# Kernel optimization log

Measured on AMD Instinct MI355X. Metric: run time of the kernel, lower is better.

Reference implementation:

```python
import jax, jax.numpy as jnp
import numpy as np

EPS = 1e-5       # norm_eps
CHUNK = 64       # scan checkpoint chunk size

def _short_conv(x, w):
    # causal depthwise conv (kernel K) + SiLU; x:[B,T,C], w:[C,K]
    K = w.shape[1]
    T = x.shape[1]
    xp = jnp.pad(x, ((0, 0), (K - 1, 0), (0, 0)))
    y = sum(xp[:, i:i + T, :] * w[:, i] for i in range(K))
    return jax.nn.silu(y)

def _l2norm(x):
    return x * jax.lax.rsqrt(jnp.sum(x * x, -1, keepdims=True) + 1e-6)

def _forward(hidden_states, Wq, Wk, Wv, conv_q, conv_k, conv_v, Wf1, Wf2, Wb,
             A_log, dt_bias, Wg, bg, o_norm_w, Wo):
    B, T, _ = hidden_states.shape
    H = A_log.shape[0]
    x = hidden_states
    q = _short_conv(x @ Wq, conv_q)
    k = _short_conv(x @ Wk, conv_k)
    v = _short_conv(x @ Wv, conv_v)
    Dk = q.shape[-1] // H
    Dv = v.shape[-1] // H
    q = _l2norm(q.reshape(B, T, H, Dk))
    k = _l2norm(k.reshape(B, T, H, Dk))
    v = v.reshape(B, T, H, Dv)
    beta = jax.nn.sigmoid(x @ Wb)                               # [B,T,H]
    g = ((x @ Wf1) @ Wf2).reshape(B, T, H, Dk)
    # KDA gate: g = -exp(A_log) * softplus(g + dt_bias), per head & key channel
    g = -jnp.exp(A_log)[:, None] * jax.nn.softplus(g + dt_bias.reshape(H, Dk))
    gexp = jnp.exp(g)                                           # decay in (0,1)
    scale = Dk ** -0.5

    def step(S, inp):
        q_t, k_t, v_t, ge_t, b_t = inp                          # [B,H,Dk]..., [B,H]
        S = S * ge_t[..., None]                                 # per-key-channel decay
        kv = jnp.einsum('bhk,bhkv->bhv', k_t, S)                # current prediction
        upd = (v_t - kv) * b_t[..., None]                       # delta-rule update
        S = S + jnp.einsum('bhk,bhv->bhkv', k_t, upd)
        o_t = jnp.einsum('bhk,bhkv->bhv', q_t, S) * scale
        return S, o_t

    @jax.checkpoint
    def chunk_fn(S, chunk):
        return jax.lax.scan(step, S, chunk)

    def tm(a):  # [B,T,...] -> [T//CHUNK, CHUNK, B, ...]
        a = jnp.moveaxis(a, 1, 0)
        return a.reshape((T // CHUNK, CHUNK) + a.shape[1:])

    S0 = jnp.zeros((B, H, Dk, Dv), dtype=q.dtype)
    _, o = jax.lax.scan(chunk_fn, S0, (tm(q), tm(k), tm(v), tm(gexp), tm(beta)))
    o = jnp.moveaxis(o.reshape((T, B, H, Dv)), 0, 1)            # [B,T,H,Dv]

    gate_o = (x @ Wg + bg).reshape(B, T, H, Dv)
    on = o * jax.lax.rsqrt(jnp.mean(o * o, -1, keepdims=True) + EPS) * o_norm_w
    on = on * jax.nn.silu(gate_o)                               # gated RMSNorm
    return on.reshape(B, T, H * Dv) @ Wo


def setup_inputs() -> dict:
    key = jax.random.key(0)
    ks = jax.random.split(key, 16)
    B, T, D = 2, 2048, 2048
    H, Dk, Dv, K = 16, 128, 128, 4
    n = jax.random.normal
    return {
        'hidden_states': n(ks[0], (B, T, D), jnp.float32),
        'Wq': n(ks[1], (D, H * Dk), jnp.float32) * D ** -0.5,
        'Wk': n(ks[2], (D, H * Dk), jnp.float32) * D ** -0.5,
        'Wv': n(ks[3], (D, H * Dv), jnp.float32) * D ** -0.5,
        'conv_q': n(ks[4], (H * Dk, K), jnp.float32) * 0.5,
        'conv_k': n(ks[5], (H * Dk, K), jnp.float32) * 0.5,
        'conv_v': n(ks[6], (H * Dv, K), jnp.float32) * 0.5,
        'Wf1': n(ks[7], (D, Dv), jnp.float32) * D ** -0.5,
        'Wf2': n(ks[8], (Dv, H * Dk), jnp.float32) * Dv ** -0.5,
        'Wb': n(ks[9], (D, H), jnp.float32) * D ** -0.5,
        'A_log': jnp.log(jax.random.uniform(ks[10], (H,), jnp.float32, 1.0, 16.0)),
        'dt_bias': jnp.zeros((H * Dk,), jnp.float32),
        'Wg': n(ks[11], (D, H * Dv), jnp.float32) * D ** -0.5,
        'bg': jnp.zeros((H * Dv,), jnp.float32),
        'o_norm_w': jnp.ones((Dv,), jnp.float32),
        'Wo': n(ks[12], (H * Dv, D), jnp.float32) * (H * Dv) ** -0.5,
    }


def reference(hidden_states, Wq, Wk, Wv, conv_q, conv_k, conv_v, Wf1, Wf2, Wb,
              A_log, dt_bias, Wg, bg, o_norm_w, Wo):
    return _forward(hidden_states, Wq, Wk, Wv, conv_q, conv_k, conv_v, Wf1, Wf2,
                    Wb, A_log, dt_bias, Wg, bg, o_norm_w, Wo)
```

## Files before the change

### kernel.cpp

```cpp
#include <hip/hip_runtime.h>
#include <stdint.h>

#define BB 2
#define TT 2048
#define DD 2048
#define HH 16
#define HD 2048
#define MM 4096
#define SCH 16

typedef float f32x4 __attribute__((ext_vector_type(4)));
typedef __bf16 bf16x8 __attribute__((ext_vector_type(8)));
typedef unsigned short u16x4 __attribute__((ext_vector_type(4)));
typedef unsigned int u32x4 __attribute__((ext_vector_type(4)));

__device__ __forceinline__ unsigned short f2b(float f) {
  unsigned int u = __float_as_uint(f);
  u += 0x7FFFu + ((u >> 16) & 1u);
  return (unsigned short)(u >> 16);
}

__device__ __forceinline__ void async_ld16(const void* g, void* l) {
  typedef __attribute__((address_space(3))) void as3_t;
  typedef const __attribute__((address_space(1))) void as1_t;
  __builtin_amdgcn_global_load_lds((as1_t*)(uintptr_t)g,
                                   (as3_t*)(unsigned int)(uintptr_t)l, 16, 0, 0);
}

template <int CTRL>
__device__ __forceinline__ float dpp_add(float x) {
  int y = __builtin_amdgcn_update_dpp(0, __float_as_int(x), CTRL, 0xF, 0xF, false);
  return x + __int_as_float(y);
}
__device__ __forceinline__ float reduce16(float x) {
  x = dpp_add<0xB1>(x);
  x = dpp_add<0x4E>(x);
  x = dpp_add<0x124>(x);
  x = dpp_add<0x128>(x);
  return x;
}

__global__ __launch_bounds__(256) void cast_f32_bf16(const float* __restrict__ in,
                                                     unsigned short* __restrict__ out,
                                                     int n4) {
  int i = blockIdx.x * 256 + threadIdx.x;
  if (i >= n4) return;
  f32x4 v = *(const f32x4*)(in + (size_t)i * 4);
  u16x4 r;
  #pragma unroll
  for (int j = 0; j < 4; j++) r[j] = f2b(v[j]);
  *(u16x4*)(out + (size_t)i * 4) = r;
}

__global__ __launch_bounds__(256) void transpose_cast(const float* __restrict__ in,
                                                      unsigned short* __restrict__ out,
                                                      int R, int C) {
  __shared__ float tile[32][33];
  int bx = blockIdx.x * 32, by = blockIdx.y * 32;
  int tx = threadIdx.x, ty = threadIdx.y;
  #pragma unroll
  for (int i = 0; i < 32; i += 8)
    tile[ty + i][tx] = in[(size_t)(by + ty + i) * C + bx + tx];
  __syncthreads();
  #pragma unroll
  for (int i = 0; i < 32; i += 8)
    out[(size_t)(bx + ty + i) * R + by + tx] = f2b(tile[tx][ty + i]);
}

#define GEMM_PROLOGUE_AND_LOOP                                                         \
  __shared__ __align__(16) unsigned short As[128 * 32];                                \
  __shared__ __align__(16) unsigned short Bs[128 * 32];                                \
  int tid = threadIdx.x;                                                               \
  int l = tid & 63, w = tid >> 6;                                                      \
  int nbx = gridDim.x;                                                                 \
  int tot = nbx * gridDim.y;                                                           \
  int id = blockIdx.y * nbx + blockIdx.x;                                              \
  int nid = id;                                                                        \
  if ((tot & 7) == 0) { int per = tot >> 3; nid = (id & 7) * per + (id >> 3); }        \
  int row0 = (nid / nbx) * 128, col0 = (nid % nbx) * 128;                              \
  int wm = (w >> 1) * 64, wn = (w & 1) * 64;                                           \
  const f32x4 fz = {0.f, 0.f, 0.f, 0.f};                                               \
  f32x4 acc[4][4];                                                                     \
  _Pragma("unroll") for (int i = 0; i < 4; i++)                                        \
    _Pragma("unroll") for (int j = 0; j < 4; j++) acc[i][j] = fz;                      \
  int srow = l >> 2, skoff = (l & 3) * 8;                                              \
  int quad = l >> 4, mrow = l & 15;                                                    \
  for (int kt = 0; kt < K; kt += 32) {                                                 \
    _Pragma("unroll") for (int i = 0; i < 2; i++) {                                    \
      int c = w * 2 + i;                                                               \
      const unsigned short* gA = A + (size_t)(row0 + c * 16 + srow) * K + kt + skoff;  \
      const unsigned short* gB = Bt + (size_t)(col0 + c * 16 + srow) * K + kt + skoff; \
      async_ld16(gA, As + c * 512);                                                    \
      async_ld16(gB, Bs + c * 512);                                                    \
    }                                                                                  \
    __syncthreads();                                                                   \
    bf16x8 af[4], bfr[4];                                                              \
    _Pragma("unroll") for (int i = 0; i < 4; i++)                                      \
      af[i] = *(const bf16x8*)(As + (wm + i * 16 + mrow) * 32 + quad * 8);             \
    _Pragma("unroll") for (int j = 0; j < 4; j++)                                      \
      bfr[j] = *(const bf16x8*)(Bs + (wn + j * 16 + mrow) * 32 + quad * 8);            \
    _Pragma("unroll") for (int i = 0; i < 4; i++)                                      \
      _Pragma("unroll") for (int j = 0; j < 4; j++)                                    \
        acc[i][j] = __builtin_amdgcn_mfma_f32_16x16x32_bf16(af[i], bfr[j], acc[i][j],  \
                                                            0, 0, 0);                  \
    __syncthreads();                                                                   \
  }

__global__ __launch_bounds__(256) void gemm_bf16(const unsigned short* __restrict__ A,
                                                 const unsigned short* __restrict__ Bt,
                                                 float* __restrict__ C,
                                                 const float* __restrict__ bias,
                                                 int M, int N, int K) {
  GEMM_PROLOGUE_AND_LOOP
  #pragma unroll
  for (int i = 0; i < 4; i++)
    #pragma unroll
    for (int j = 0; j < 4; j++)
      #pragma unroll
      for (int r = 0; r < 4; r++) {
        int rr = row0 + wm + i * 16 + quad * 4 + r;
        int cc = col0 + wn + j * 16 + mrow;
        float v = acc[i][j][r];
        if (bias) v += bias[cc];
        C[(size_t)rr * N + cc] = v;
      }
}

__global__ __launch_bounds__(256) void gemm_bf16_bout(const unsigned short* __restrict__ A,
                                                      const unsigned short* __restrict__ Bt,
                                                      unsigned short* __restrict__ C,
                                                      const float* __restrict__ bias,
                                                      int M, int N, int K) {
  GEMM_PROLOGUE_AND_LOOP
  #pragma unroll
  for (int i = 0; i < 4; i++)
    #pragma unroll
    for (int j = 0; j < 4; j++)
      #pragma unroll
      for (int r = 0; r < 4; r++) {
        int rr = row0 + wm + i * 16 + quad * 4 + r;
        int cc = col0 + wn + j * 16 + mrow;
        C[(size_t)rr * N + cc] = f2b(acc[i][j][r] + bias[cc]);
      }
}

__global__ __launch_bounds__(256) void gemm_qkv(const unsigned short* __restrict__ A,
                                                const unsigned short* __restrict__ Bt,
                                                unsigned short* __restrict__ Dq,
                                                unsigned short* __restrict__ Dk,
                                                unsigned short* __restrict__ Dv,
                                                int M, int N, int K) {
  GEMM_PROLOGUE_AND_LOOP
  {
    int cc0 = col0 + wn + mrow;
    (void)cc0;
  }
  #pragma unroll
  for (int i = 0; i < 4; i++)
    #pragma unroll
    for (int j = 0; j < 4; j++)
      #pragma unroll
      for (int r = 0; r < 4; r++) {
        int rr = row0 + wm + i * 16 + quad * 4 + r;
        int cc = col0 + wn + j * 16 + mrow;
        int sub = cc >> 11;
        int ch = cc & (HD - 1);
        int h = ch >> 7, c2 = ch & 127;
        int b = rr >> 11, t = rr & (TT - 1);
        unsigned short* dst = (sub == 0) ? Dq : (sub == 1) ? Dk : Dv;
        dst[(((size_t)(b * HH + h)) * TT + t) * 128 + c2] = f2b(acc[i][j][r]);
      }
}

__global__ __launch_bounds__(256) void conv_silu_kernel(const unsigned short* __restrict__ Pre,
                                                        const float* __restrict__ cw,
                                                        float* __restrict__ outp,
                                                        int do_norm, float post_mul) {
  int bt = blockIdx.x;
  int b = bt >> 11, t = bt & (TT - 1);
  int tid = threadIdx.x;
  int ch0 = tid * 8;
  int h = tid >> 4, c0 = (tid & 15) * 8;
  f32x4 wv[8];
  #pragma unroll
  for (int j = 0; j < 8; j++) wv[j] = *(const f32x4*)(cw + (size_t)(ch0 + j) * 4);
  float acc[8] = {0, 0, 0, 0, 0, 0, 0, 0};
  const unsigned short* base = Pre + (((size_t)(b * HH + h)) * TT) * 128 + c0;
  #pragma unroll
  for (int i = 0; i < 4; i++) {
    int tt = t - 3 + i;
    if (tt < 0) continue;
    u32x4 raw = *(const u32x4*)(base + (size_t)tt * 128);
    float e[8];
    #pragma unroll
    for (int jj = 0; jj < 4; jj++) {
      e[2 * jj]     = __uint_as_float(raw[jj] << 16);
      e[2 * jj + 1] = __uint_as_float(raw[jj] & 0xffff0000u);
    }
    #pragma unroll
    for (int j = 0; j < 8; j++) acc[j] += e[j] * wv[j][i];
  }
  float val[8];
  #pragma unroll
  for (int j = 0; j < 8; j++) val[j] = acc[j] / (1.f + expf(-acc[j]));
  if (do_norm) {
    float ss = 0.f;
    #pragma unroll
    for (int j = 0; j < 8; j++) ss += val[j] * val[j];
    ss = reduce16(ss);
    float rs = rsqrtf(ss + 1e-6f) * post_mul;
    #pragma unroll
    for (int j = 0; j < 8; j++) val[j] *= rs;
  }
  float* op = outp + (((size_t)(b * HH + h)) * TT + t) * 128 + c0;
  f32x4 o0, o1;
  #pragma unroll
  for (int j = 0; j < 4; j++) { o0[j] = val[j]; o1[j] = val[4 + j]; }
  *(f32x4*)op = o0;
  *(f32x4*)(op + 4) = o1;
}

__global__ __launch_bounds__(256) void beta_kernel(const float* __restrict__ x,
                                                   const float* __restrict__ Wb,
                                                   float* __restrict__ beta) {
  __shared__ float xs[2048];
  int bt = blockIdx.x, tid = threadIdx.x;
  int b = bt >> 11, t = bt & (TT - 1);
  const float* row = x + (size_t)bt * DD;
  #pragma unroll
  for (int i = 0; i < 2; i++)
    *(f32x4*)(xs + tid * 8 + i * 4) = *(const f32x4*)(row + tid * 8 + i * 4);
  __syncthreads();
  int h = tid >> 4, seg = tid & 15;
  float p = 0.f;
  for (int j = 0; j < 128; j++) {
    int d = seg * 128 + ((j + seg * 9) & 127);
    p += xs[d] * Wb[(size_t)d * HH + h];
  }
  p = reduce16(p);
  if (seg == 0) beta[((size_t)(b * HH + h)) * TT + t] = 1.f / (1.f + expf(-p));
}

__global__ __launch_bounds__(256) void gexp_kernel(const float* __restrict__ g,
                                                   const float* __restrict__ A_log,
                                                   const float* __restrict__ dt_bias,
                                                   float* __restrict__ ge, int n) {
  int i = blockIdx.x * 256 + threadIdx.x;
  if (i >= n) return;
  int bt = i >> 11, ch = i & (HD - 1);
  int b = bt >> 11, t = bt & (TT - 1);
  int h = ch >> 7, c = ch & 127;
  float gv = g[i] + dt_bias[ch];
  float sp = (gv > 20.f) ? gv : log1pf(expf(gv));
  ge[(((size_t)(b * HH + h)) * TT + t) * 128 + c] = expf(-expf(A_log[h]) * sp);
}

__global__ __launch_bounds__(256, 1) void scan_kernel(const float* __restrict__ q,
                                                      const float* __restrict__ k,
                                                      const float* v,
                                                      const float* __restrict__ ge,
                                                      const float* __restrict__ beta,
                                                      float* o) {
  __shared__ __align__(16) float kbuf[2][SCH * 128];
  __shared__ __align__(16) float gbuf[2][SCH * 128];
  __shared__ __align__(16) float qbuf[2][SCH * 128];
  __shared__ __align__(16) float vbuf[2][SCH * 16];
  __shared__ __align__(16) float bbuf[TT];

  int blk = blockIdx.x;
  int bh = blk & 31;
  int colblk = blk >> 5;
  int tid = threadIdx.x;
  int w = tid >> 6, l = tid & 63;
  int grp = l >> 4, i = l & 15;
  int lcol = w * 4 + grp;
  int col = colblk * 16 + lcol;

  int par = grp & 1;
  int of0 = (2 * i + par) * 4;
  int of1 = (2 * i + (1 - par)) * 4;

  const float* kbh = k    + (size_t)bh * TT * 128;
  const float* gbh = ge   + (size_t)bh * TT * 128;
  const float* qbh = q    + (size_t)bh * TT * 128;
  const float* vbh = v    + (size_t)bh * TT * 128;
  const float* bbh = beta + (size_t)bh * TT;
  float* obh = o + (size_t)bh * TT * 128;

  #pragma unroll
  for (int j = 0; j < 2; j++) {
    int jj = w * 2 + j;
    async_ld16(bbh + jj * 256 + l * 4, (float*)bbuf + jj * 256);
  }
  auto stage = [&](int cidx, int nb) {
    size_t t0 = (size_t)cidx * SCH;
    if (w == 0) {
      #pragma unroll
      for (int j = 0; j < 8; j++)
        async_ld16(kbh + t0 * 128 + j * 256 + l * 4, (float*)kbuf[nb] + j * 256);
    } else if (w == 1) {
      #pragma unroll
      for (int j = 0; j < 8; j++)
        async_ld16(gbh + t0 * 128 + j * 256 + l * 4, (float*)gbuf[nb] + j * 256);
    } else if (w == 2) {
      #pragma unroll
      for (int j = 0; j < 8; j++)
        async_ld16(qbh + t0 * 128 + j * 256 + l * 4, (float*)qbuf[nb] + j * 256);
    } else {
      async_ld16(vbh + (t0 + (size_t)(l >> 2)) * 128 + colblk * 16 + (l & 3) * 4,
                 (float*)vbuf[nb]);
    }
  };
  stage(0, 0);
  __syncthreads();

  f32x4 s0 = {0.f, 0.f, 0.f, 0.f}, s1 = {0.f, 0.f, 0.f, 0.f};
  float okeep = 0.f;

  for (int c = 0; c < TT / SCH; c++) {
    int cb = c & 1, nb = cb ^ 1;
    if (c + 1 < TT / SCH) stage(c + 1, nb);

    const float* kc = (const float*)kbuf[cb];
    const float* gc = (const float*)gbuf[cb];
    const float* qc = (const float*)qbuf[cb];
    float vbt[SCH], btp[SCH];
    #pragma unroll
    for (int s = 0; s < SCH; s++) {
      float vv = ((const float*)vbuf[cb])[s * 16 + lcol];
      float bb = bbuf[c * SCH + s];
      btp[s] = bb;
      vbt[s] = vv * bb;
    }
    f32x4 k0 = *(const f32x4*)(kc + of0), k1 = *(const f32x4*)(kc + of1);
    f32x4 g0 = *(const f32x4*)(gc + of0), g1 = *(const f32x4*)(gc + of1);
    f32x4 q0 = *(const f32x4*)(qc + of0), q1 = *(const f32x4*)(qc + of1);
    #pragma unroll
    for (int s = 0; s < SCH; s++) {
      f32x4 k0n, k1n, g0n, g1n, q0n, q1n;
      if (s + 1 < SCH) {
        const float* kp = kc + (s + 1) * 128;
        const float* gp = gc + (s + 1) * 128;
        const float* qp = qc + (s + 1) * 128;
        k0n = *(const f32x4*)(kp + of0); k1n = *(const f32x4*)(kp + of1);
        g0n = *(const f32x4*)(gp + of0); g1n = *(const f32x4*)(gp + of1);
        q0n = *(const f32x4*)(qp + of0); q1n = *(const f32x4*)(qp + of1);
      }
      f32x4 kg0 = k0 * g0, kg1 = k1 * g1;
      f32x4 pp = kg0 * s0 + kg1 * s1;
      float p = (pp[0] + pp[1]) + (pp[2] + pp[3]);
      p = reduce16(p);
      s0 *= g0; s1 *= g1;
      float u = fmaf(-btp[s], p, vbt[s]);
      s0 += k0 * u; s1 += k1 * u;
      f32x4 oo = q0 * s0 + q1 * s1;
      float po = (oo[0] + oo[1]) + (oo[2] + oo[3]);
      po = reduce16(po);
      okeep = (i == s) ? po : okeep;
      if (s + 1 < SCH) {
        k0 = k0n; k1 = k1n; g0 = g0n; g1 = g1n; q0 = q0n; q1 = q1n;
      }
    }
    obh[((size_t)c * SCH + i) * 128 + col] = okeep;
    __syncthreads();
  }
}

__global__ __launch_bounds__(256) void out_norm_kernel(const float* o,
                                                       const unsigned short* __restrict__ gate,
                                                       const float* __restrict__ w,
                                                       unsigned short* __restrict__ onb) {
  int bt = blockIdx.x, tid = threadIdx.x;
  int b = bt >> 11, t = bt & (TT - 1);
  int h = tid >> 4, seg = tid & 15;
  size_t obase = (((size_t)(b * HH + h)) * TT + t) * 128 + seg * 8;
  size_t gbase = (size_t)bt * HD + (size_t)h * 128 + seg * 8;
  f32x4 o0 = *(const f32x4*)(o + obase);
  f32x4 o1 = *(const f32x4*)(o + obase + 4);
  u32x4 graw = *(const u32x4*)(gate + gbase);
  float gv[8];
  #pragma unroll
  for (int jj = 0; jj < 4; jj++) {
    gv[2 * jj]     = __uint_as_float(graw[jj] << 16);
    gv[2 * jj + 1] = __uint_as_float(graw[jj] & 0xffff0000u);
  }
  float ss = 0.f;
  #pragma unroll
  for (int j = 0; j < 4; j++) ss += o0[j] * o0[j] + o1[j] * o1[j];
  ss = reduce16(ss);
  float rs = rsqrtf(ss * (1.f / 128.f) + 1e-5f);
  u16x4 r0, r1;
  #pragma unroll
  for (int j = 0; j < 4; j++) {
    float gv0 = gv[j];
    float gv1 = gv[4 + j];
    float a0 = o0[j] * rs * w[seg * 8 + j] * (gv0 / (1.f + expf(-gv0)));
    float a1 = o1[j] * rs * w[seg * 8 + 4 + j] * (gv1 / (1.f + expf(-gv1)));
    r0[j] = f2b(a0);
    r1[j] = f2b(a1);
  }
  *(u16x4*)(onb + gbase) = r0;
  *(u16x4*)(onb + gbase + 4) = r1;
}

extern "C" void kernel_launch(void* const* d_in, const int* in_sizes, int n_in,
                              void* d_out, int out_size, void* d_ws, size_t ws_size,
                              hipStream_t stream) {
  const float* x       = (const float*)d_in[0];
  const float* Wq      = (const float*)d_in[1];
  const float* Wk      = (const float*)d_in[2];
  const float* Wv      = (const float*)d_in[3];
  const float* cq      = (const float*)d_in[4];
  const float* ck      = (const float*)d_in[5];
  const float* cv      = (const float*)d_in[6];
  const float* Wf1     = (const float*)d_in[7];
  const float* Wf2     = (const float*)d_in[8];
  const float* Wb      = (const float*)d_in[9];
  const float* A_log   = (const float*)d_in[10];
  const float* dt_bias = (const float*)d_in[11];
  const float* Wg      = (const float*)d_in[12];
  const float* bg      = (const float*)d_in[13];
  const float* onw     = (const float*)d_in[14];
  const float* Wo      = (const float*)d_in[15];
  float* out = (float*)d_out;

  char* ws = (char*)d_ws;
  unsigned short* WT  = (unsigned short*)(ws);
  unsigned short* xb  = (unsigned short*)(ws + ((size_t)24 << 20));
  float* geb          = (float*)(ws + ((size_t)40 << 20));
  float* P2           = (float*)(ws + ((size_t)72 << 20));
  unsigned short* B1  = (unsigned short*)(ws + ((size_t)72 << 20));
  unsigned short* B2  = (unsigned short*)(ws + ((size_t)88 << 20));
  unsigned short* B3  = (unsigned short*)(ws + ((size_t)104 << 20));
  float* qc           = (float*)(ws + ((size_t)120 << 20));
  float* kc           = (float*)(ws + ((size_t)152 << 20));
  float* vc           = (float*)(ws + ((size_t)72 << 20));
  unsigned short* gateb = (unsigned short*)(ws + ((size_t)104 << 20));
  float* f1           = (float*)(ws + ((size_t)184 << 20));
  unsigned short* f1b = (unsigned short*)(ws + ((size_t)186 << 20));
  float* betab        = (float*)(ws + ((size_t)187 << 20));
  unsigned short* onb = xb;
  float* ob = vc;

  dim3 tb(32, 8);

  cast_f32_bf16<<<(MM * DD / 4 + 255) / 256, 256, 0, stream>>>(x, xb, MM * DD / 4);

  transpose_cast<<<dim3(128 / 32, DD / 32), tb, 0, stream>>>(Wf1, WT, DD, 128);
  gemm_bf16<<<dim3(1, MM / 128), 256, 0, stream>>>(xb, WT, f1, nullptr, MM, 128, DD);
  cast_f32_bf16<<<(MM * 128 / 4 + 255) / 256, 256, 0, stream>>>(f1, f1b, MM * 128 / 4);
  transpose_cast<<<dim3(HD / 32, 128 / 32), tb, 0, stream>>>(Wf2, WT, 128, HD);
  gemm_bf16<<<dim3(HD / 128, MM / 128), 256, 0, stream>>>(f1b, WT, P2, nullptr, MM, HD, 128);
  gexp_kernel<<<(MM * HD + 255) / 256, 256, 0, stream>>>(P2, A_log, dt_bias, geb, MM * HD);

  beta_kernel<<<MM, 256, 0, stream>>>(x, Wb, betab);

  transpose_cast<<<dim3(HD / 32, DD / 32), tb, 0, stream>>>(Wq, WT, DD, HD);
  transpose_cast<<<dim3(HD / 32, DD / 32), tb, 0, stream>>>(Wk, WT + (size_t)2048 * 2048, DD, HD);
  transpose_cast<<<dim3(HD / 32, DD / 32), tb, 0, stream>>>(Wv, WT + (size_t)4096 * 2048, DD, HD);

  gemm_qkv<<<dim3(6144 / 128, MM / 128), 256, 0, stream>>>(xb, WT, B1, B2, B3, MM, 6144, DD);

  conv_silu_kernel<<<MM, 256, 0, stream>>>(B1, cq, qc, 1, 0.08838834764831845f);
  conv_silu_kernel<<<MM, 256, 0, stream>>>(B2, ck, kc, 1, 1.0f);
  conv_silu_kernel<<<MM, 256, 0, stream>>>(B3, cv, vc, 0, 1.0f);

  transpose_cast<<<dim3(HD / 32, DD / 32), tb, 0, stream>>>(Wg, WT, DD, HD);
  gemm_bf16_bout<<<dim3(HD / 128, MM / 128), 256, 0, stream>>>(xb, WT, gateb, bg, MM, HD, DD);

  scan_kernel<<<BB * HH * 8, 256, 0, stream>>>(qc, kc, vc, geb, betab, ob);

  out_norm_kernel<<<MM, 256, 0, stream>>>(ob, gateb, onw, onb);

  transpose_cast<<<dim3(DD / 32, HD / 32), tb, 0, stream>>>(Wo, WT, HD, DD);
  gemm_bf16<<<dim3(DD / 128, MM / 128), 256, 0, stream>>>(onb, WT, out, nullptr, MM, DD, HD);
}
```

Baseline: 1.152 ms.

## Fuse gate GEMM into QKV GEMM, fuse gexp epilogue, store q/k as bf16

Merges the gate projection into the QKV GEMM (N=8192 with a bias epilogue for the gate slice). It also folds the softplus/exp decay computation into the Wf2 GEMM epilogue, which removes the fp32 P2 round trip and a separate kernel. The conv kernels now write q and k in bf16, and the scan kernel stages them in bf16 with duplicated LDS copies that replace the old parity-based offsets. This cuts memory traffic and launches, at the cost of lower precision for q and k inside the recurrent scan.

```diff
diff --git a/kernel.cpp b/kernel.cpp
--- a/kernel.cpp
+++ b/kernel.cpp
@@ -18,6 +18,13 @@
   unsigned int u = __float_as_uint(f);
   u += 0x7FFFu + ((u >> 16) & 1u);
   return (unsigned short)(u >> 16);
+}
+
+__device__ __forceinline__ void unpack8(u32x4 r, f32x4& lo, f32x4& hi) {
+  lo[0] = __uint_as_float(r[0] << 16); lo[1] = __uint_as_float(r[0] & 0xffff0000u);
+  lo[2] = __uint_as_float(r[1] << 16); lo[3] = __uint_as_float(r[1] & 0xffff0000u);
+  hi[0] = __uint_as_float(r[2] << 16); hi[1] = __uint_as_float(r[2] & 0xffff0000u);
+  hi[2] = __uint_as_float(r[3] << 16); hi[3] = __uint_as_float(r[3] & 0xffff0000u);
 }
 
 __device__ __forceinline__ void async_ld16(const void* g, void* l) {
@@ -126,35 +133,15 @@
       }
 }
 
-__global__ __launch_bounds__(256) void gemm_bf16_bout(const unsigned short* __restrict__ A,
-                                                      const unsigned short* __restrict__ Bt,
-                                                      unsigned short* __restrict__ C,
-                                                      const float* __restrict__ bias,
-                                                      int M, int N, int K) {
+__global__ __launch_bounds__(256) void gemm_qkvg(const unsigned short* __restrict__ A,
+                                                 const unsigned short* __restrict__ Bt,
+                                                 unsigned short* __restrict__ Dq,
+                                                 unsigned short* __restrict__ Dk,
+                                                 unsigned short* __restrict__ Dv,
+                                                 unsigned short* __restrict__ Dg,
+                                                 const float* __restrict__ bg,
+                                                 int M, int N, int K) {
   GEMM_PROLOGUE_AND_LOOP
-  #pragma unroll
-  for (int i = 0; i < 4; i++)
-    #pragma unroll
-    for (int j = 0; j < 4; j++)
-      #pragma unroll
-      for (int r = 0; r < 4; r++) {
-        int rr = row0 + wm + i * 16 + quad * 4 + r;
-        int cc = col0 + wn + j * 16 + mrow;
-        C[(size_t)rr * N + cc] = f2b(acc[i][j][r] + bias[cc]);
-      }
-}
-
-__global__ __launch_bounds__(256) void gemm_qkv(const unsigned short* __restrict__ A,
-                                                const unsigned short* __restrict__ Bt,
-                                                unsigned short* __restrict__ Dq,
-                                                unsigned short* __restrict__ Dk,
-                                                unsigned short* __restrict__ Dv,
-                                                int M, int N, int K) {
-  GEMM_PROLOGUE_AND_LOOP
-  {
-    int cc0 = col0 + wn + mrow;
-    (void)cc0;
-  }
   #pragma unroll
   for (int i = 0; i < 4; i++)
     #pragma unroll
@@ -165,17 +152,47 @@
         int cc = col0 + wn + j * 16 + mrow;
         int sub = cc >> 11;
         int ch = cc & (HD - 1);
-        int h = ch >> 7, c2 = ch & 127;
         int b = rr >> 11, t = rr & (TT - 1);
-        unsigned short* dst = (sub == 0) ? Dq : (sub == 1) ? Dk : Dv;
-        dst[(((size_t)(b * HH + h)) * TT + t) * 128 + c2] = f2b(acc[i][j][r]);
+        if (sub == 3) {
+          Dg[(size_t)rr * HD + ch] = f2b(acc[i][j][r] + bg[ch]);
+        } else {
+          int h = ch >> 7, c2 = ch & 127;
+          unsigned short* dst = (sub == 0) ? Dq : (sub == 1) ? Dk : Dv;
+          dst[(((size_t)(b * HH + h)) * TT + t) * 128 + c2] = f2b(acc[i][j][r]);
+        }
+      }
+}
+
+__global__ __launch_bounds__(256) void gemm_gexp(const unsigned short* __restrict__ A,
+                                                 const unsigned short* __restrict__ Bt,
+                                                 float* __restrict__ GE,
+                                                 const float* __restrict__ A_log,
+                                                 const float* __restrict__ dt_bias,
+                                                 int M, int N, int K) {
+  GEMM_PROLOGUE_AND_LOOP
+  int h = col0 >> 7;
+  float Ae = expf(A_log[h]);
+  #pragma unroll
+  for (int i = 0; i < 4; i++)
+    #pragma unroll
+    for (int j = 0; j < 4; j++)
+      #pragma unroll
+      for (int r = 0; r < 4; r++) {
+        int rr = row0 + wm + i * 16 + quad * 4 + r;
+        int cc = col0 + wn + j * 16 + mrow;
+        int b = rr >> 11, t = rr & (TT - 1);
+        int c2 = cc & 127;
+        float gv = acc[i][j][r] + dt_bias[cc];
+        float sp = (gv > 20.f) ? gv : log1pf(expf(gv));
+        GE[(((size_t)(b * HH + h)) * TT + t) * 128 + c2] = expf(-Ae * sp);
       }
 }
 
 __global__ __launch_bounds__(256) void conv_silu_kernel(const unsigned short* __restrict__ Pre,
                                                         const float* __restrict__ cw,
-                                                        float* __restrict__ outp,
-                                                        int do_norm, float post_mul) {
+                                                        void* __restrict__ outp,
+                                                        int do_norm, float post_mul,
+                                                        int obf16) {
   int bt = blockIdx.x;
   int b = bt >> 11, t = bt & (TT - 1);
   int tid = threadIdx.x;
@@ -212,12 +229,22 @@
     #pragma unroll
     for (int j = 0; j < 8; j++) val[j] *= rs;
   }
-  float* op = outp + (((size_t)(b * HH + h)) * TT + t) * 128 + c0;
-  f32x4 o0, o1;
-  #pragma unroll
-  for (int j = 0; j < 4; j++) { o0[j] = val[j]; o1[j] = val[4 + j]; }
-  *(f32x4*)op = o0;
-  *(f32x4*)(op + 4) = o1;
+  size_t idx = (((size_t)(b * HH + h)) * TT + t) * 128 + c0;
+  if (obf16) {
+    unsigned short* op = (unsigned short*)outp + idx;
+    u16x4 r0, r1;
+    #pragma unroll
+    for (int j = 0; j < 4; j++) { r0[j] = f2b(val[j]); r1[j] = f2b(val[4 + j]); }
+    *(u16x4*)op = r0;
+    *(u16x4*)(op + 4) = r1;
+  } else {
+    float* op = (float*)outp + idx;
+    f32x4 o0, o1;
+    #pragma unroll
+    for (int j = 0; j < 4; j++) { o0[j] = val[j]; o1[j] = val[4 + j]; }
+    *(f32x4*)op = o0;
+    *(f32x4*)(op + 4) = o1;
+  }
 }
 
 __global__ __launch_bounds__(256) void beta_kernel(const float* __restrict__ x,
@@ -241,29 +268,15 @@
   if (seg == 0) beta[((size_t)(b * HH + h)) * TT + t] = 1.f / (1.f + expf(-p));
 }
 
-__global__ __launch_bounds__(256) void gexp_kernel(const float* __restrict__ g,
-                                                   const float* __restrict__ A_log,
-                                                   const float* __restrict__ dt_bias,
-                                                   float* __restrict__ ge, int n) {
-  int i = blockIdx.x * 256 + threadIdx.x;
-  if (i >= n) return;
-  int bt = i >> 11, ch = i & (HD - 1);
-  int b = bt >> 11, t = bt & (TT - 1);
-  int h = ch >> 7, c = ch & 127;
-  float gv = g[i] + dt_bias[ch];
-  float sp = (gv > 20.f) ? gv : log1pf(expf(gv));
-  ge[(((size_t)(b * HH + h)) * TT + t) * 128 + c] = expf(-expf(A_log[h]) * sp);
-}
-
-__global__ __launch_bounds__(256, 1) void scan_kernel(const float* __restrict__ q,
-                                                      const float* __restrict__ k,
-                                                      const float* v,
+__global__ __launch_bounds__(256, 1) void scan_kernel(const unsigned short* __restrict__ q,
+                                                      const unsigned short* __restrict__ k,
+                                                      const float* __restrict__ v,
                                                       const float* __restrict__ ge,
                                                       const float* __restrict__ beta,
-                                                      float* o) {
-  __shared__ __align__(16) float kbuf[2][SCH * 128];
-  __shared__ __align__(16) float gbuf[2][SCH * 128];
-  __shared__ __align__(16) float qbuf[2][SCH * 128];
+                                                      float* __restrict__ o) {
+  __shared__ __align__(16) float gbuf[2][2 * SCH * 128];
+  __shared__ __align__(16) unsigned short kbuf[2][2 * SCH * 128];
+  __shared__ __align__(16) unsigned short qbuf[2][2 * SCH * 128];
   __shared__ __align__(16) float vbuf[2][SCH * 16];
   __shared__ __align__(16) float bbuf[TT];
 
@@ -275,15 +288,12 @@
   int grp = l >> 4, i = l & 15;
   int lcol = w * 4 + grp;
   int col = colblk * 16 + lcol;
-
-  int par = grp & 1;
-  int of0 = (2 * i + par) * 4;
-  int of1 = (2 * i + (1 - par)) * 4;
-
-  const float* kbh = k    + (size_t)bh * TT * 128;
-  const float* gbh = ge   + (size_t)bh * TT * 128;
-  const float* qbh = q    + (size_t)bh * TT * 128;
-  const float* vbh = v    + (size_t)bh * TT * 128;
+  int copy = grp & 1;
+
+  const unsigned short* kbh = k + (size_t)bh * TT * 128;
+  const unsigned short* qbh = q + (size_t)bh * TT * 128;
+  const float* gbh = ge + (size_t)bh * TT * 128;
+  const float* vbh = v + (size_t)bh * TT * 128;
   const float* bbh = beta + (size_t)bh * TT;
   float* obh = o + (size_t)bh * TT * 128;
 
@@ -297,16 +307,30 @@
     if (w == 0) {
       #pragma unroll
       for (int j = 0; j < 8; j++)
-        async_ld16(kbh + t0 * 128 + j * 256 + l * 4, (float*)kbuf[nb] + j * 256);
+        async_ld16(gbh + t0 * 128 + j * 256 + l * 4, (float*)gbuf[nb] + j * 256);
     } else if (w == 1) {
       #pragma unroll
       for (int j = 0; j < 8; j++)
-        async_ld16(gbh + t0 * 128 + j * 256 + l * 4, (float*)gbuf[nb] + j * 256);
+        async_ld16(gbh + t0 * 128 + j * 256 + l * 4,
+                   (float*)gbuf[nb] + SCH * 128 + j * 256);
     } else if (w == 2) {
       #pragma unroll
-      for (int j = 0; j < 8; j++)
-        async_ld16(qbh + t0 * 128 + j * 256 + l * 4, (float*)qbuf[nb] + j * 256);
+      for (int j = 0; j < 4; j++)
+        async_ld16(kbh + t0 * 128 + j * 512 + l * 8,
+                   (unsigned short*)kbuf[nb] + j * 512);
+      #pragma unroll
+      for (int j = 0; j < 4; j++)
+        async_ld16(kbh + t0 * 128 + j * 512 + l * 8,
+                   (unsigned short*)kbuf[nb] + SCH * 128 + j * 512);
     } else {
+      #pragma unroll
+      for (int j = 0; j < 4; j++)
+        async_ld16(qbh + t0 * 128 + j * 512 + l * 8,
+                   (unsigned short*)qbuf[nb] + j * 512);
+      #pragma unroll
+      for (int j = 0; j < 4; j++)
+        async_ld16(qbh + t0 * 128 + j * 512 + l * 8,
+                   (unsigned short*)qbuf[nb] + SCH * 128 + j * 512);
       async_ld16(vbh + (t0 + (size_t)(l >> 2)) * 128 + colblk * 16 + (l & 3) * 4,
                  (float*)vbuf[nb]);
     }
@@ -321,31 +345,33 @@
     int cb = c & 1, nb = cb ^ 1;
     if (c + 1 < TT / SCH) stage(c + 1, nb);
 
-    const float* kc = (const float*)kbuf[cb];
-    const float* gc = (const float*)gbuf[cb];
-    const float* qc = (const float*)qbuf[cb];
+    const unsigned short* kcp = kbuf[cb] + copy * (SCH * 128);
+    const unsigned short* qcp = qbuf[cb] + copy * (SCH * 128);
+    const float* gcp = gbuf[cb] + copy * (SCH * 128);
+
     float vbt[SCH], btp[SCH];
     #pragma unroll
     for (int s = 0; s < SCH; s++) {
-      float vv = ((const float*)vbuf[cb])[s * 16 + lcol];
+      float vv = vbuf[cb][s * 16 + lcol];
       float bb = bbuf[c * SCH + s];
       btp[s] = bb;
       vbt[s] = vv * bb;
     }
-    f32x4 k0 = *(const f32x4*)(kc + of0), k1 = *(const f32x4*)(kc + of1);
-    f32x4 g0 = *(const f32x4*)(gc + of0), g1 = *(const f32x4*)(gc + of1);
-    f32x4 q0 = *(const f32x4*)(qc + of0), q1 = *(const f32x4*)(qc + of1);
+    u32x4 kr = *(const u32x4*)(kcp + i * 8);
+    u32x4 qr = *(const u32x4*)(qcp + i * 8);
+    f32x4 g0 = *(const f32x4*)(gcp + i * 8), g1 = *(const f32x4*)(gcp + i * 8 + 4);
     #pragma unroll
     for (int s = 0; s < SCH; s++) {
-      f32x4 k0n, k1n, g0n, g1n, q0n, q1n;
+      u32x4 krn, qrn; f32x4 g0n, g1n;
       if (s + 1 < SCH) {
-        const float* kp = kc + (s + 1) * 128;
-        const float* gp = gc + (s + 1) * 128;
-        const float* qp = qc + (s + 1) * 128;
-        k0n = *(const f32x4*)(kp + of0); k1n = *(const f32x4*)(kp + of1);
-        g0n = *(const f32x4*)(gp + of0); g1n = *(const f32x4*)(gp + of1);
-        q0n = *(const f32x4*)(qp + of0); q1n = *(const f32x4*)(qp + of1);
+        krn = *(const u32x4*)(kcp + (s + 1) * 128 + i * 8);
+        qrn = *(const u32x4*)(qcp + (s + 1) * 128 + i * 8);
+        g0n = *(const f32x4*)(gcp + (s + 1) * 128 + i * 8);
+        g1n = *(const f32x4*)(gcp + (s + 1) * 128 + i * 8 + 4);
       }
+      f32x4 k0, k1, q0, q1;
+      unpack8(kr, k0, k1);
+      unpack8(qr, q0, q1);
       f32x4 kg0 = k0 * g0, kg1 = k1 * g1;
       f32x4 pp = kg0 * s0 + kg1 * s1;
       float p = (pp[0] + pp[1]) + (pp[2] + pp[3]);
@@ -357,16 +383,14 @@
       float po = (oo[0] + oo[1]) + (oo[2] + oo[3]);
       po = reduce16(po);
       okeep = (i == s) ? po : okeep;
-      if (s + 1 < SCH) {
-        k0 = k0n; k1 = k1n; g0 = g0n; g1 = g1n; q0 = q0n; q1 = q1n;
-      }
+      if (s + 1 < SCH) { kr = krn; qr = qrn; g0 = g0n; g1 = g1n; }
     }
     obh[((size_t)c * SCH + i) * 128 + col] = okeep;
     __syncthreads();
   }
 }
 
-__global__ __launch_bounds__(256) void out_norm_kernel(const float* o,
+__global__ __launch_bounds__(256) void out_norm_kernel(const float* __restrict__ o,
                                                        const unsigned short* __restrict__ gate,
                                                        const float* __restrict__ w,
                                                        unsigned short* __restrict__ onb) {
@@ -425,22 +449,21 @@
   float* out = (float*)d_out;
 
   char* ws = (char*)d_ws;
-  unsigned short* WT  = (unsigned short*)(ws);
-  unsigned short* xb  = (unsigned short*)(ws + ((size_t)24 << 20));
-  float* geb          = (float*)(ws + ((size_t)40 << 20));
-  float* P2           = (float*)(ws + ((size_t)72 << 20));
-  unsigned short* B1  = (unsigned short*)(ws + ((size_t)72 << 20));
-  unsigned short* B2  = (unsigned short*)(ws + ((size_t)88 << 20));
-  unsigned short* B3  = (unsigned short*)(ws + ((size_t)104 << 20));
-  float* qc           = (float*)(ws + ((size_t)120 << 20));
-  float* kc           = (float*)(ws + ((size_t)152 << 20));
-  float* vc           = (float*)(ws + ((size_t)72 << 20));
-  unsigned short* gateb = (unsigned short*)(ws + ((size_t)104 << 20));
-  float* f1           = (float*)(ws + ((size_t)184 << 20));
-  unsigned short* f1b = (unsigned short*)(ws + ((size_t)186 << 20));
-  float* betab        = (float*)(ws + ((size_t)187 << 20));
-  unsigned short* onb = xb;
-  float* ob = vc;
+  unsigned short* WT    = (unsigned short*)(ws);
+  unsigned short* xb    = (unsigned short*)(ws + ((size_t)32 << 20));
+  float* geb            = (float*)(ws + ((size_t)48 << 20));
+  unsigned short* B1    = (unsigned short*)(ws + ((size_t)80 << 20));
+  unsigned short* B2    = (unsigned short*)(ws + ((size_t)96 << 20));
+  unsigned short* B3    = (unsigned short*)(ws + ((size_t)112 << 20));
+  unsigned short* gateb = (unsigned short*)(ws + ((size_t)128 << 20));
+  unsigned short* kc16  = (unsigned short*)(ws + ((size_t)144 << 20));
+  float* f1             = (float*)(ws + ((size_t)160 << 20));
+  unsigned short* f1b   = (unsigned short*)(ws + ((size_t)162 << 20));
+  float* betab          = (float*)(ws + ((size_t)163 << 20));
+  unsigned short* qc16  = xb;
+  float* vc             = (float*)(ws + ((size_t)80 << 20));
+  float* ob             = vc;
+  unsigned short* onb   = B3;
 
   dim3 tb(32, 8);
 
@@ -450,25 +473,24 @@
   gemm_bf16<<<dim3(1, MM / 128), 256, 0, stream>>>(xb, WT, f1, nullptr, MM, 128, DD);
   cast_f32_bf16<<<(MM * 128 / 4 + 255) / 256, 256, 0, stream>>>(f1, f1b, MM * 128 / 4);
   transpose_cast<<<dim3(HD / 32, 128 / 32), tb, 0, stream>>>(Wf2, WT, 128, HD);
-  gemm_bf16<<<dim3(HD / 128, MM / 128), 256, 0, stream>>>(f1b, WT, P2, nullptr, MM, HD, 128);
-  gexp_kernel<<<(MM * HD + 255) / 256, 256, 0, stream>>>(P2, A_log, dt_bias, geb, MM * HD);
+  gemm_gexp<<<dim3(HD / 128, MM / 128), 256, 0, stream>>>(f1b, WT, geb, A_log, dt_bias,
+                                                          MM, HD, 128);
 
   beta_kernel<<<MM, 256, 0, stream>>>(x, Wb, betab);
 
   transpose_cast<<<dim3(HD / 32, DD / 32), tb, 0, stream>>>(Wq, WT, DD, HD);
   transpose_cast<<<dim3(HD / 32, DD / 32), tb, 0, stream>>>(Wk, WT + (size_t)2048 * 2048, DD, HD);
   transpose_cast<<<dim3(HD / 32, DD / 32), tb, 0, stream>>>(Wv, WT + (size_t)4096 * 2048, DD, HD);
-
-  gemm_qkv<<<dim3(6144 / 128, MM / 128), 256, 0, stream>>>(xb, WT, B1, B2, B3, MM, 6144, DD);
-
-  conv_silu_kernel<<<MM, 256, 0, stream>>>(B1, cq, qc, 1, 0.08838834764831845f);
-  conv_silu_kernel<<<MM, 256, 0, stream>>>(B2, ck, kc, 1, 1.0f);
-  conv_silu_kernel<<<MM, 256, 0, stream>>>(B3, cv, vc, 0, 1.0f);
-
-  transpose_cast<<<dim3(HD / 32, DD / 32), tb, 0, stream>>>(Wg, WT, DD, HD);
-  gemm_bf16_bout<<<dim3(HD / 128, MM / 128), 256, 0, stream>>>(xb, WT, gateb, bg, MM, HD, DD);
-
-  scan_kernel<<<BB * HH * 8, 256, 0, stream>>>(qc, kc, vc, geb, betab, ob);
+  transpose_cast<<<dim3(HD / 32, DD / 32), tb, 0, stream>>>(Wg, WT + (size_t)6144 * 2048, DD, HD);
+
+  gemm_qkvg<<<dim3(8192 / 128, MM / 128), 256, 0, stream>>>(xb, WT, B1, B2, B3,
+                                                            gateb, bg, MM, 8192, DD);
+
+  conv_silu_kernel<<<MM, 256, 0, stream>>>(B1, cq, qc16, 1, 0.08838834764831845f, 1);
+  conv_silu_kernel<<<MM, 256, 0, stream>>>(B2, ck, kc16, 1, 1.0f, 1);
+  conv_silu_kernel<<<MM, 256, 0, stream>>>(B3, cv, vc,   0, 1.0f, 0);
+
+  scan_kernel<<<BB * HH * 8, 256, 0, stream>>>(qc16, kc16, vc, geb, betab, ob);
 
   out_norm_kernel<<<MM, 256, 0, stream>>>(ob, gateb, onw, onb);
 
```

After: 1.194 ms. 1.04x slower.
